# Optimization experiments

Hardware: AMD Instinct MI355X
Metric: run time of the kernel (lower is better)

Reference implementation:

```python
import jax, jax.numpy as jnp
import numpy as np

N_VARS = 50000
N_CLAUSES = 200000
E = 800000
D = 128
NFC = 3
ROUNDS = 16


def setup_inputs() -> dict:
    key = jax.random.key(0)
    ks = jax.random.split(key, 20)
    s = 0.05
    inp = {
        'L_init_w': jax.random.normal(ks[0], (D, 1)) * s,
        'L_init_b': jax.random.normal(ks[1], (D,)) * s,
        'C_init_w': jax.random.normal(ks[2], (D, 1)) * s,
        'C_init_b': jax.random.normal(ks[3], (D,)) * s,
        'Lmsg_w': jax.random.normal(ks[4], (NFC, D, D)) * s,
        'Lmsg_b': jax.random.normal(ks[5], (NFC, D)) * s,
        'Cmsg_w': jax.random.normal(ks[6], (NFC, D, D)) * s,
        'Cmsg_b': jax.random.normal(ks[7], (NFC, D)) * s,
        'Cu_wih': jax.random.normal(ks[8], (4 * D, D)) * s,
        'Cu_whh': jax.random.normal(ks[9], (4 * D, D)) * s,
        'Cu_bih': jax.random.normal(ks[10], (4 * D,)) * s,
        'Cu_bhh': jax.random.normal(ks[11], (4 * D,)) * s,
        'Lu_wih': jax.random.normal(ks[12], (4 * D, 2 * D)) * s,
        'Lu_whh': jax.random.normal(ks[13], (4 * D, D)) * s,
        'Lu_bih': jax.random.normal(ks[14], (4 * D,)) * s,
        'Lu_bhh': jax.random.normal(ks[15], (4 * D,)) * s,
        # bipartite CNF edges: src = literal index in [0, 2*n_vars), dst = local clause id in [0, n_clauses)
        'edge_src': jax.random.randint(ks[16], (E,), 0, 2 * N_VARS),
        'edge_dst': jax.random.randint(ks[17], (E,), 0, N_CLAUSES),
        'n_vars': N_VARS,
        'n_clauses': N_CLAUSES,
        'num_rounds': ROUNDS,
    }
    return inp


def _mlp(x, ws, bs):
    n = ws.shape[0]
    for i in range(n):
        x = x @ ws[i].T + bs[i]
        if i < n - 1:
            x = jax.nn.relu(x)
    return x


def _lstm(x, h, c, wih, whh, bih, bhh):
    g = x @ wih.T + h @ whh.T + bih + bhh
    i, f, gg, o = jnp.split(g, 4, axis=-1)
    c2 = jax.nn.sigmoid(f) * c + jax.nn.sigmoid(i) * jnp.tanh(gg)
    return jax.nn.sigmoid(o) * jnp.tanh(c2), c2


def reference(L_init_w, L_init_b, C_init_w, C_init_b, Lmsg_w, Lmsg_b, Cmsg_w, Cmsg_b,
              Cu_wih, Cu_whh, Cu_bih, Cu_bhh, Lu_wih, Lu_whh, Lu_bih, Lu_bhh,
              edge_src, edge_dst, n_vars, n_clauses, num_rounds):
    d = L_init_b.shape[0]
    V2 = 2 * n_vars              # literals occupy [0, V2)
    N = V2 + n_clauses           # clauses occupy [V2, N)
    l_vec = L_init_w[:, 0] + L_init_b   # L_init(ones(1))
    c_vec = C_init_w[:, 0] + C_init_b   # C_init(ones(1))
    h = jnp.concatenate([jnp.broadcast_to(l_vec, (V2, d)),
                         jnp.broadcast_to(c_vec, (n_clauses, d))], axis=0)
    c = jnp.zeros((N, d), h.dtype)

    def body(carry, _):
        h, c = carry
        # literal -> clause messages (deepset: sum of MLP(h_lit) over clause neighborhood)
        lm = _mlp(h[:V2], Lmsg_w, Lmsg_b)                          # [V2, d]
        c_msg = jax.ops.segment_sum(lm[edge_src], edge_dst, num_segments=n_clauses)
        hc, cc = _lstm(c_msg, h[V2:], c[V2:], Cu_wih, Cu_whh, Cu_bih, Cu_bhh)
        h = h.at[V2:].set(hc)
        c = c.at[V2:].set(cc)
        # clause -> literal messages (reverse direction)
        cm = _mlp(h[V2:], Cmsg_w, Cmsg_b)                          # [n_clauses, d]
        l_msg = jax.ops.segment_sum(cm[edge_dst], edge_src, num_segments=V2)
        # literal flip: state of the negated literal
        l_neg = jnp.concatenate([h[n_vars:V2], h[:n_vars]], axis=0)
        hl, cl = _lstm(jnp.concatenate([l_msg, l_neg], axis=1), h[:V2], c[:V2],
                       Lu_wih, Lu_whh, Lu_bih, Lu_bhh)
        h = h.at[:V2].set(hl)
        c = c.at[:V2].set(cl)
        return (h, c), None

    (h, c), _ = jax.lax.scan(body, (h, c), None, length=num_rounds)
    return h
```

## Files before the change

### kernel.cpp

```cpp
#include <hip/hip_runtime.h>
#include <stdint.h>

#define NVARS  50000
#define NLIT   100000
#define NCLS   200000
#define NNODE  300000
#define NEDGE  800000
#define DD     128
#define NROUNDS 16
#define NSEG   300000
#define CSRN   1600000

typedef __attribute__((ext_vector_type(8))) short   short8;
typedef __attribute__((ext_vector_type(4))) float   floatx4;

typedef __attribute__((address_space(1))) const void gvoid_t;
typedef __attribute__((address_space(3))) void       svoid_t;

static __device__ __forceinline__ float bf2f(uint16_t u){
  union { uint32_t i; float f; } v; v.i = ((uint32_t)u) << 16; return v.f;
}
static __device__ __forceinline__ uint16_t f2bf(float f){
  union { float f; uint32_t i; } v; v.f = f;
  uint32_t x = v.i;
  return (uint16_t)((x + 0x7fffu + ((x >> 16) & 1u)) >> 16);
}
static __device__ __forceinline__ float sane(float x){ return (fabsf(x) < 1e30f) ? x : 0.0f; }
static __device__ __forceinline__ float sigm(float x){ return 1.0f / (1.0f + __expf(-x)); }
static __device__ __forceinline__ float tanh_f(float x){ return 1.0f - 2.0f / (__expf(2.0f*x) + 1.0f); }

__global__ void k_init(const float* __restrict__ Lw, const float* __restrict__ Lb,
                       const float* __restrict__ Cw, const float* __restrict__ Cb,
                       uint16_t* __restrict__ hb, float* __restrict__ c32){
  long tid = (long)blockIdx.x*256 + threadIdx.x;
  if (tid >= (long)NNODE*DD) return;
  int d = (int)(tid & (DD-1));
  long i = tid >> 7;
  float v = (i < NLIT) ? (Lw[d] + Lb[d]) : (Cw[d] + Cb[d]);
  hb[tid] = f2bf(v);
  c32[tid] = 0.0f;
}

__global__ void k_setup(const float* __restrict__ Cu_wih, const float* __restrict__ Cu_whh,
                        const float* __restrict__ Cu_bih, const float* __restrict__ Cu_bhh,
                        const float* __restrict__ Lu_wih, const float* __restrict__ Lu_whh,
                        const float* __restrict__ Lu_bih, const float* __restrict__ Lu_bhh,
                        uint16_t* __restrict__ Wc, uint16_t* __restrict__ Wl,
                        float* __restrict__ bsc, float* __restrict__ bsl){
  int n = blockIdx.x;
  int t = threadIdx.x;
  Wc[n*256 + t]       = f2bf(Cu_wih[n*128 + t]);
  Wc[n*256 + 128 + t] = f2bf(Cu_whh[n*128 + t]);
  Wl[n*384 + t]       = f2bf(Lu_wih[n*256 + t]);
  Wl[n*384 + 128 + t] = f2bf(Lu_wih[n*256 + 128 + t]);
  Wl[n*384 + 256 + t] = f2bf(Lu_whh[n*128 + t]);
  if (t == 0){
    bsc[n] = Cu_bih[n] + Cu_bhh[n];
    bsl[n] = Lu_bih[n] + Lu_bhh[n];
  }
}

__global__ void k_cvtmsg(const float* __restrict__ LmW, const float* __restrict__ CmW,
                         uint16_t* __restrict__ LmWb, uint16_t* __restrict__ CmWb){
  int i = blockIdx.x*256 + threadIdx.x;
  if (i < 49152)            LmWb[i]         = f2bf(LmW[i]);
  else if (i < 2*49152)     CmWb[i - 49152] = f2bf(CmW[i - 49152]);
}

__global__ void k_hist(const int* esrc, const int* edst, int* cnt){
  int e = blockIdx.x*256 + threadIdx.x; if (e >= NEDGE) return;
  int s = esrc[e], d = edst[e];
  if ((unsigned)d < (unsigned)NCLS) atomicAdd(&cnt[d], 1);
  if ((unsigned)s < (unsigned)NLIT) atomicAdd(&cnt[NCLS + s], 1);
}

__global__ void k_reduce(const int* cnt, int* part){
  __shared__ int sm[1024];
  int i = blockIdx.x*1024 + threadIdx.x;
  sm[threadIdx.x] = (i < NSEG) ? cnt[i] : 0;
  __syncthreads();
  for (int s = 512; s > 0; s >>= 1){
    if (threadIdx.x < s) sm[threadIdx.x] += sm[threadIdx.x + s];
    __syncthreads();
  }
  if (threadIdx.x == 0) part[blockIdx.x] = sm[0];
}

__global__ void k_scanpart(int* part, int nb){
  if (blockIdx.x == 0 && threadIdx.x == 0){
    int s = 0;
    for (int b = 0; b < nb; ++b){ int v = part[b]; part[b] = s; s += v; }
  }
}

__global__ void k_scanapply(const int* cnt, const int* part, int* off, int* cur){
  __shared__ int sm[1024];
  int i = blockIdx.x*1024 + threadIdx.x;
  int v = (i < NSEG) ? cnt[i] : 0;
  sm[threadIdx.x] = v;
  __syncthreads();
  for (int s = 1; s < 1024; s <<= 1){
    int t = (threadIdx.x >= s) ? sm[threadIdx.x - s] : 0;
    __syncthreads();
    sm[threadIdx.x] += t;
    __syncthreads();
  }
  if (i < NSEG){
    int excl = part[blockIdx.x] + sm[threadIdx.x] - v;
    off[i] = excl; cur[i] = excl;
    if (i == NSEG-1) off[NSEG] = excl + v;
  }
}

__global__ void k_scatter(const int* esrc, const int* edst, int* cur, int* csr){
  int e = blockIdx.x*256 + threadIdx.x; if (e >= NEDGE) return;
  int s = esrc[e], d = edst[e];
  if ((unsigned)s < (unsigned)NLIT && (unsigned)d < (unsigned)NCLS){
    int p  = atomicAdd(&cur[d], 1);        if ((unsigned)p  < (unsigned)CSRN) csr[p]  = s;
    int p2 = atomicAdd(&cur[NCLS + s], 1); if ((unsigned)p2 < (unsigned)CSRN) csr[p2] = d;
  }
}

__global__ void k_segsum(const uint16_t* __restrict__ rows, int rowsN,
                         uint16_t* __restrict__ out,
                         const int* __restrict__ off, const int* __restrict__ csr,
                         int nseg, int segbase){
  int seg = blockIdx.x*4 + (threadIdx.x >> 6);
  if (seg >= nseg) return;
  int lane = threadIdx.x & 63;
  int s0 = off[segbase + seg], s1 = off[segbase + seg + 1];
  if (s0 < 0) s0 = 0;
  if (s1 > CSRN) s1 = CSRN;
  float ax = 0.f, ay = 0.f;
  for (int e = s0; e < s1; ++e){
    unsigned idx = (unsigned)csr[e];
    if (idx >= (unsigned)rowsN) idx = 0;
    uint32_t v = *reinterpret_cast<const uint32_t*>(rows + (size_t)idx*DD + lane*2);
    ax += bf2f((uint16_t)(v & 0xffffu));
    ay += bf2f((uint16_t)(v >> 16));
  }
  ax = sane(ax); ay = sane(ay);
  *reinterpret_cast<uint32_t*>(out + (size_t)seg*DD + lane*2) =
      (uint32_t)f2bf(ax) | ((uint32_t)f2bf(ay) << 16);
}

__global__ void __launch_bounds__(512, 4)
k_mlp3(const uint16_t* __restrict__ A, const uint16_t* __restrict__ W,
       const float* __restrict__ bias, uint16_t* __restrict__ out, int M){
  __shared__ uint16_t sX[8192];
  __shared__ uint16_t sY[8192];
  int tid  = threadIdx.x;
  int wv   = tid >> 6, lane = tid & 63;
  int mrow = lane & 15, qq = lane >> 4;
  int r0   = blockIdx.x*64;
  int slot = qq ^ ((mrow >> 1) & 3);
  int j    = wv*16 + mrow;

  short8 bfr[3][4];
#pragma unroll
  for (int l = 0; l < 3; ++l)
#pragma unroll
    for (int kt = 0; kt < 4; ++kt)
      bfr[l][kt] = *reinterpret_cast<const short8*>(
          W + (size_t)l*16384 + (size_t)j*DD + kt*32 + qq*8);

#pragma unroll
  for (int p = 0; p < 2; ++p){
    int chunk = p*512 + tid;
    int kt  = chunk >> 8;
    int row = (chunk >> 2) & 63;
    int c   = chunk & 3;
    int qc  = c ^ ((row >> 1) & 3);
    long r  = r0 + row; if (r > M-1) r = M-1;
    const uint16_t* src = A + (size_t)r*DD + kt*32 + qc*8;
    __builtin_amdgcn_global_load_lds((gvoid_t*)src,
                                     (svoid_t*)&sX[(size_t)(p*512 + wv*64)*8],
                                     16, 0, 0);
  }

  int ktj = j >> 5;
  int qcj = (j >> 3) & 3;
  __syncthreads();

  uint16_t* sIn  = sX;
  uint16_t* sOut = sY;
#pragma unroll
  for (int l = 0; l < 3; ++l){
    float bv = bias[l*128 + j];
    floatx4 acc[4];
#pragma unroll
    for (int mi = 0; mi < 4; ++mi){ floatx4 z = {0.f,0.f,0.f,0.f}; acc[mi] = z; }
#pragma unroll
    for (int kt = 0; kt < 4; ++kt)
#pragma unroll
      for (int mi = 0; mi < 4; ++mi){
        short8 af = *reinterpret_cast<const short8*>(
            &sIn[(size_t)((kt*64 + mi*16 + mrow)*4 + slot)*8]);
        acc[mi] = __builtin_amdgcn_mfma_f32_16x16x32_bf16(af, bfr[l][kt], acc[mi], 0, 0, 0);
      }
    if (l < 2){
#pragma unroll
      for (int mi = 0; mi < 4; ++mi)
#pragma unroll
        for (int r2 = 0; r2 < 4; ++r2){
          int row = mi*16 + qq*4 + r2;
          float v = sane(acc[mi][r2] + bv);
          v = v > 0.f ? v : 0.f;
          int s = qcj ^ ((row >> 1) & 3);
          sOut[(size_t)((ktj*64 + row)*4 + s)*8 + (j & 7)] = f2bf(v);
        }
      __syncthreads();
      uint16_t* t = sIn; sIn = sOut; sOut = t;
    } else {
#pragma unroll
      for (int mi = 0; mi < 4; ++mi)
#pragma unroll
        for (int r2 = 0; r2 < 4; ++r2){
          int row = r0 + mi*16 + qq*4 + r2;
          float v = sane(acc[mi][r2] + bv);
          if (row < M) out[(size_t)row*DD + j] = f2bf(v);
        }
    }
  }
}

template<int K, int NEG1>
__global__ void __launch_bounds__(512, 4)
k_lstm_fused(const uint16_t* __restrict__ A0, const uint16_t* __restrict__ A1,
             const uint16_t* __restrict__ A2,
             const uint16_t* __restrict__ W, const float* __restrict__ bias,
             float* __restrict__ c32, uint16_t* __restrict__ hout, int M){
  constexpr int NT = K/32;
  __shared__ uint16_t sW[2][16384];
  __shared__ uint16_t sA[2][2048];

  int tid  = threadIdx.x;
  int wv   = tid >> 6, lane = tid & 63;
  int mrow = lane & 15, qq = lane >> 4;
  int fb   = wv;
  int r0   = blockIdx.x*64;
  int wvu  = __builtin_amdgcn_readfirstlane(wv);

  int slot = qq ^ ((mrow >> 1) & 3);
  int sq   = (lane & 3) ^ ((lane >> 3) & 3);
  int srow = wv*16 + (lane >> 2);
  int alr  = (wv & 3)*16 + (lane >> 2);

  floatx4 acc[4][4];
#pragma unroll
  for (int i = 0; i < 4; ++i)
#pragma unroll
    for (int j = 0; j < 4; ++j){ floatx4 z = {0.f,0.f,0.f,0.f}; acc[i][j] = z; }

  auto stage = [&](int buf, int tn){
    int kt = tn*32;
#pragma unroll
    for (int c = 0; c < 4; ++c){
      const uint16_t* src = W + (size_t)(srow + c*128)*K + kt + sq*8;
      __builtin_amdgcn_global_load_lds((gvoid_t*)src,
                                       (svoid_t*)&sW[buf][wv*512 + c*4096],
                                       16, 0, 0);
    }
    if (wvu < 4){
      int rg = tn >> 2;
      const uint16_t* Ar = (rg == 0) ? A0 : ((rg == 1) ? A1 : A2);
      long gr = r0 + alr; if (gr > M-1) gr = M-1;
      if (NEG1 && rg == 1) gr = (gr < NVARS) ? gr + NVARS : gr - NVARS;
      const uint16_t* asrc = Ar + (size_t)gr*DD + (tn & 3)*32 + sq*8;
      __builtin_amdgcn_global_load_lds((gvoid_t*)asrc,
                                       (svoid_t*)&sA[buf][wv*512],
                                       16, 0, 0);
    }
  };

  stage(0, 0);
  asm volatile("s_waitcnt vmcnt(0)" ::: "memory");
  __builtin_amdgcn_sched_barrier(0);
  __builtin_amdgcn_s_barrier();
  __builtin_amdgcn_sched_barrier(0);

#pragma unroll
  for (int t = 0; t < NT; ++t){
    const int cur = t & 1;
    if (t + 1 < NT){
      stage(cur ^ 1, t + 1);
      if (wvu < 4) asm volatile("s_waitcnt vmcnt(5)" ::: "memory");
      else         asm volatile("s_waitcnt vmcnt(4)" ::: "memory");
    } else {
      asm volatile("s_waitcnt vmcnt(0)" ::: "memory");
    }
    __builtin_amdgcn_sched_barrier(0);
    __builtin_amdgcn_s_barrier();
    __builtin_amdgcn_sched_barrier(0);

    short8 af[4], bf[4];
#pragma unroll
    for (int mi = 0; mi < 4; ++mi)
      af[mi] = *reinterpret_cast<const short8*>(&sA[cur][(mi*16 + mrow)*32 + slot*8]);
#pragma unroll
    for (int gg = 0; gg < 4; ++gg)
      bf[gg] = *reinterpret_cast<const short8*>(&sW[cur][(gg*128 + fb*16 + mrow)*32 + slot*8]);
#pragma unroll
    for (int mi = 0; mi < 4; ++mi)
#pragma unroll
      for (int gg = 0; gg < 4; ++gg)
        acc[mi][gg] = __builtin_amdgcn_mfma_f32_16x16x32_bf16(af[mi], bf[gg], acc[mi][gg], 0, 0, 0);

    asm volatile("s_waitcnt lgkmcnt(0)" ::: "memory");
    __builtin_amdgcn_sched_barrier(0);
    __builtin_amdgcn_s_barrier();
    __builtin_amdgcn_sched_barrier(0);
  }

  int j = fb*16 + mrow;
  float bi = bias[j], bfv = bias[j+128], bg = bias[j+256], bo = bias[j+384];
#pragma unroll
  for (int mi = 0; mi < 4; ++mi){
    floatx4 vi = acc[mi][0], vf = acc[mi][1], vg = acc[mi][2], vo = acc[mi][3];
#pragma unroll
    for (int r2 = 0; r2 < 4; ++r2){
      int row = r0 + mi*16 + qq*4 + r2;
      if (row < M){
        size_t ix = (size_t)row*DD + j;
        float iv = sane(vi[r2] + bi);
        float fv = sane(vf[r2] + bfv);
        float gv = sane(vg[r2] + bg);
        float ov = sane(vo[r2] + bo);
        float c0 = sane(c32[ix]);
        float c2 = sigm(fv)*c0 + sigm(iv)*tanh_f(gv);
        c32[ix]  = c2;
        hout[ix] = f2bf(sigm(ov)*tanh_f(c2));
      }
    }
  }
}

__global__ void k_copy16(const uint16_t* __restrict__ src, uint16_t* __restrict__ dst, long n8){
  long i = (long)blockIdx.x*256 + threadIdx.x;
  if (i >= n8) return;
  *reinterpret_cast<ulonglong2*>(dst + i*8) =
      *reinterpret_cast<const ulonglong2*>(src + i*8);
}

__global__ void k_final(const uint16_t* __restrict__ hb, float* __restrict__ out){
  long i = (long)blockIdx.x*256 + threadIdx.x;
  if (i >= (long)NNODE*DD/4) return;
  ushort4 v = *reinterpret_cast<const ushort4*>(hb + i*4);
  float4 o;
  o.x = bf2f(v.x); o.y = bf2f(v.y); o.z = bf2f(v.z); o.w = bf2f(v.w);
  *reinterpret_cast<float4*>(out + i*4) = o;
}

extern "C" void kernel_launch(void* const* d_in, const int* in_sizes, int n_in,
                              void* d_out, int out_size, void* d_ws, size_t ws_size,
                              hipStream_t stream){
  const float* Lw     = (const float*)d_in[0];
  const float* Lb     = (const float*)d_in[1];
  const float* Cw     = (const float*)d_in[2];
  const float* Cb     = (const float*)d_in[3];
  const float* LmW    = (const float*)d_in[4];
  const float* LmB    = (const float*)d_in[5];
  const float* CmW    = (const float*)d_in[6];
  const float* CmB    = (const float*)d_in[7];
  const float* Cu_wih = (const float*)d_in[8];
  const float* Cu_whh = (const float*)d_in[9];
  const float* Cu_bih = (const float*)d_in[10];
  const float* Cu_bhh = (const float*)d_in[11];
  const float* Lu_wih = (const float*)d_in[12];
  const float* Lu_whh = (const float*)d_in[13];
  const float* Lu_bih = (const float*)d_in[14];
  const float* Lu_bhh = (const float*)d_in[15];
  const int* esrc = (const int*)d_in[16];
  const int* edst = (const int*)d_in[17];

  char* p = (char*)d_ws;
  auto alloc = [&](size_t bytes)->char* {
    char* r = p; p += (bytes + 255) & ~(size_t)255; return r;
  };
  int* cnt  = (int*)alloc((size_t)NSEG*4);
  int* off  = (int*)alloc((size_t)(NSEG+1)*4);
  int* cur  = (int*)alloc((size_t)NSEG*4);
  int nb = (NSEG + 1023) / 1024;
  int* part = (int*)alloc((size_t)nb*4);
  int* csr  = (int*)alloc((size_t)CSRN*4);
  uint16_t* Wc   = (uint16_t*)alloc((size_t)512*256*2);
  uint16_t* Wl   = (uint16_t*)alloc((size_t)512*384*2);
  uint16_t* LmWb = (uint16_t*)alloc((size_t)3*128*128*2);
  uint16_t* CmWb = (uint16_t*)alloc((size_t)3*128*128*2);
  float* bsc = (float*)alloc(512*4);
  float* bsl = (float*)alloc(512*4);
  uint16_t* t0 = (uint16_t*)alloc((size_t)NCLS*DD*2);
  uint16_t* t1 = (uint16_t*)alloc((size_t)NCLS*DD*2);
  uint16_t* hb = (uint16_t*)alloc((size_t)NNODE*DD*2);

  float* c32 = (float*)d_out;
  uint16_t* hbC = hb  + (size_t)NLIT*DD;
  float*    cL  = c32;
  float*    cC  = c32 + (size_t)NLIT*DD;

  hipMemsetAsync(cnt, 0, (size_t)NSEG*4, stream);
  k_init<<<(NNODE*DD + 255)/256, 256, 0, stream>>>(Lw, Lb, Cw, Cb, hb, c32);
  k_setup<<<512, 128, 0, stream>>>(Cu_wih, Cu_whh, Cu_bih, Cu_bhh,
                                   Lu_wih, Lu_whh, Lu_bih, Lu_bhh,
                                   Wc, Wl, bsc, bsl);
  k_cvtmsg<<<(2*49152 + 255)/256, 256, 0, stream>>>(LmW, CmW, LmWb, CmWb);
  k_hist<<<(NEDGE + 255)/256, 256, 0, stream>>>(esrc, edst, cnt);
  k_reduce<<<nb, 1024, 0, stream>>>(cnt, part);
  k_scanpart<<<1, 64, 0, stream>>>(part, nb);
  k_scanapply<<<nb, 1024, 0, stream>>>(cnt, part, off, cur);
  k_scatter<<<(NEDGE + 255)/256, 256, 0, stream>>>(esrc, edst, cur, csr);

  for (int rd = 0; rd < NROUNDS; ++rd){
    k_mlp3<<<1563, 512, 0, stream>>>(hb, LmWb, LmB, t0, NLIT);
    k_segsum<<<50000, 256, 0, stream>>>(t0, NLIT, t1, off, csr, NCLS, 0);
    k_lstm_fused<256,0><<<3125, 512, 0, stream>>>(t1, hbC, nullptr, Wc, bsc, cC, hbC, NCLS);
    k_mlp3<<<3125, 512, 0, stream>>>(hbC, CmWb, CmB, t0, NCLS);
    k_segsum<<<25000, 256, 0, stream>>>(t0, NCLS, t1, off, csr, NLIT, NCLS);
    k_copy16<<<6250, 256, 0, stream>>>(hb, t0, (long)NLIT*DD/8);
    k_lstm_fused<384,1><<<1563, 512, 0, stream>>>(t1, t0, t0, Wl, bsl, cL, hb, NLIT);
  }

  k_final<<<(NNODE*DD/4 + 255)/256, 256, 0, stream>>>(hb, (float*)d_out);
}
```

Before: 9.488 ms.

## Pair literal and negation rows in LSTM tile; keep clause LSTM weights in registers

The literal LSTM kernel now gives each block 32 variables plus their 32 negated literals. The negation input is then always a row inside the same block's update set, so the per-round copy of literal h into a scratch buffer is dropped and the kernel reads and writes hb in place. The clause LSTM kernel drops its LDS double-buffered pipeline and keeps its full weight slice in registers, loading activations straight from global memory. The in-place update assumes no block reads rows another block writes, which this pairing ensures. The register-resident weights raise register pressure, and the launch-bounds occupancy hint drops from 4 to 2.

```diff
diff --git a/kernel.cpp b/kernel.cpp
--- a/kernel.cpp
+++ b/kernel.cpp
@@ -224,93 +224,53 @@
   }
 }
 
-template<int K, int NEG1>
-__global__ void __launch_bounds__(512, 4)
-k_lstm_fused(const uint16_t* __restrict__ A0, const uint16_t* __restrict__ A1,
-             const uint16_t* __restrict__ A2,
-             const uint16_t* __restrict__ W, const float* __restrict__ bias,
-             float* __restrict__ c32, uint16_t* __restrict__ hout, int M){
-  constexpr int NT = K/32;
-  __shared__ uint16_t sW[2][16384];
-  __shared__ uint16_t sA[2][2048];
-
+__global__ void __launch_bounds__(512, 2)
+k_lstm_cls(const uint16_t* __restrict__ A0, const uint16_t* __restrict__ A1,
+           const uint16_t* __restrict__ W, const float* __restrict__ bias,
+           float* __restrict__ c32, uint16_t* __restrict__ hout, int M){
   int tid  = threadIdx.x;
   int wv   = tid >> 6, lane = tid & 63;
   int mrow = lane & 15, qq = lane >> 4;
   int fb   = wv;
   int r0   = blockIdx.x*64;
-  int wvu  = __builtin_amdgcn_readfirstlane(wv);
-
-  int slot = qq ^ ((mrow >> 1) & 3);
-  int sq   = (lane & 3) ^ ((lane >> 3) & 3);
-  int srow = wv*16 + (lane >> 2);
-  int alr  = (wv & 3)*16 + (lane >> 2);
+
+  short8 breg[4][8];
+#pragma unroll
+  for (int gg = 0; gg < 4; ++gg)
+#pragma unroll
+    for (int t = 0; t < 8; ++t)
+      breg[gg][t] = *reinterpret_cast<const short8*>(
+          W + (size_t)(gg*128 + fb*16 + mrow)*256 + t*32 + qq*8);
+
+  const uint16_t* ap[2][4];
+#pragma unroll
+  for (int mi = 0; mi < 4; ++mi){
+    int r = r0 + mi*16 + mrow; if (r > M-1) r = M-1;
+    ap[0][mi] = A0 + (size_t)r*DD + qq*8;
+    ap[1][mi] = A1 + (size_t)r*DD + qq*8;
+  }
 
   floatx4 acc[4][4];
 #pragma unroll
   for (int i = 0; i < 4; ++i)
 #pragma unroll
-    for (int j = 0; j < 4; ++j){ floatx4 z = {0.f,0.f,0.f,0.f}; acc[i][j] = z; }
-
-  auto stage = [&](int buf, int tn){
-    int kt = tn*32;
-#pragma unroll
-    for (int c = 0; c < 4; ++c){
-      const uint16_t* src = W + (size_t)(srow + c*128)*K + kt + sq*8;
-      __builtin_amdgcn_global_load_lds((gvoid_t*)src,
-                                       (svoid_t*)&sW[buf][wv*512 + c*4096],
-                                       16, 0, 0);
-    }
-    if (wvu < 4){
-      int rg = tn >> 2;
-      const uint16_t* Ar = (rg == 0) ? A0 : ((rg == 1) ? A1 : A2);
-      long gr = r0 + alr; if (gr > M-1) gr = M-1;
-      if (NEG1 && rg == 1) gr = (gr < NVARS) ? gr + NVARS : gr - NVARS;
-      const uint16_t* asrc = Ar + (size_t)gr*DD + (tn & 3)*32 + sq*8;
-      __builtin_amdgcn_global_load_lds((gvoid_t*)asrc,
-                                       (svoid_t*)&sA[buf][wv*512],
-                                       16, 0, 0);
-    }
-  };
-
-  stage(0, 0);
-  asm volatile("s_waitcnt vmcnt(0)" ::: "memory");
-  __builtin_amdgcn_sched_barrier(0);
-  __builtin_amdgcn_s_barrier();
-  __builtin_amdgcn_sched_barrier(0);
-
-#pragma unroll
-  for (int t = 0; t < NT; ++t){
-    const int cur = t & 1;
-    if (t + 1 < NT){
-      stage(cur ^ 1, t + 1);
-      if (wvu < 4) asm volatile("s_waitcnt vmcnt(5)" ::: "memory");
-      else         asm volatile("s_waitcnt vmcnt(4)" ::: "memory");
-    } else {
-      asm volatile("s_waitcnt vmcnt(0)" ::: "memory");
-    }
-    __builtin_amdgcn_sched_barrier(0);
-    __builtin_amdgcn_s_barrier();
-    __builtin_amdgcn_sched_barrier(0);
-
-    short8 af[4], bf[4];
+    for (int j2 = 0; j2 < 4; ++j2){ floatx4 z = {0.f,0.f,0.f,0.f}; acc[i][j2] = z; }
+
+#pragma unroll
+  for (int t = 0; t < 8; ++t){
+    const int rg = t >> 2, ko = (t & 3)*32;
+    short8 af[4];
 #pragma unroll
     for (int mi = 0; mi < 4; ++mi)
-      af[mi] = *reinterpret_cast<const short8*>(&sA[cur][(mi*16 + mrow)*32 + slot*8]);
-#pragma unroll
-    for (int gg = 0; gg < 4; ++gg)
-      bf[gg] = *reinterpret_cast<const short8*>(&sW[cur][(gg*128 + fb*16 + mrow)*32 + slot*8]);
+      af[mi] = *reinterpret_cast<const short8*>(ap[rg][mi] + ko);
 #pragma unroll
     for (int mi = 0; mi < 4; ++mi)
 #pragma unroll
       for (int gg = 0; gg < 4; ++gg)
-        acc[mi][gg] = __builtin_amdgcn_mfma_f32_16x16x32_bf16(af[mi], bf[gg], acc[mi][gg], 0, 0, 0);
-
-    asm volatile("s_waitcnt lgkmcnt(0)" ::: "memory");
-    __builtin_amdgcn_sched_barrier(0);
-    __builtin_amdgcn_s_barrier();
-    __builtin_amdgcn_sched_barrier(0);
-  }
+        acc[mi][gg] = __builtin_amdgcn_mfma_f32_16x16x32_bf16(af[mi], breg[gg][t], acc[mi][gg], 0, 0, 0);
+  }
+
+  __syncthreads();
 
   int j = fb*16 + mrow;
   float bi = bias[j], bfv = bias[j+128], bg = bias[j+256], bo = bias[j+384];
@@ -335,11 +295,122 @@
   }
 }
 
-__global__ void k_copy16(const uint16_t* __restrict__ src, uint16_t* __restrict__ dst, long n8){
-  long i = (long)blockIdx.x*256 + threadIdx.x;
-  if (i >= n8) return;
-  *reinterpret_cast<ulonglong2*>(dst + i*8) =
-      *reinterpret_cast<const ulonglong2*>(src + i*8);
+__global__ void __launch_bounds__(512, 4)
+k_lstm_lit(const uint16_t* __restrict__ A0, const uint16_t* __restrict__ hbl,
+           const uint16_t* __restrict__ W, const float* __restrict__ bias,
+           float* __restrict__ c32, uint16_t* __restrict__ hout){
+  constexpr int NT = 12;
+  __shared__ uint16_t sW[2][16384];
+  __shared__ uint16_t sA[2][2048];
+
+  int tid  = threadIdx.x;
+  int wv   = tid >> 6, lane = tid & 63;
+  int mrow = lane & 15, qq = lane >> 4;
+  int fb   = wv;
+  long base = (long)blockIdx.x*32;
+  int wvu  = __builtin_amdgcn_readfirstlane(wv);
+
+  int slot = qq ^ ((mrow >> 1) & 3);
+  int sq   = (lane & 3) ^ ((lane >> 3) & 3);
+  int srow = wv*16 + (lane >> 2);
+  int alr  = (wv & 3)*16 + (lane >> 2);
+
+  auto pmap = [&](int lr)->long {
+    long g = (lr < 32) ? base + lr : (long)NVARS + base + (lr - 32);
+    long cap = (lr < 32) ? (long)NVARS - 1 : (long)NLIT - 1;
+    return g > cap ? cap : g;
+  };
+
+  floatx4 acc[4][4];
+#pragma unroll
+  for (int i = 0; i < 4; ++i)
+#pragma unroll
+    for (int j2 = 0; j2 < 4; ++j2){ floatx4 z = {0.f,0.f,0.f,0.f}; acc[i][j2] = z; }
+
+  auto stage = [&](int buf, int tn){
+    int kt = tn*32;
+#pragma unroll
+    for (int c = 0; c < 4; ++c){
+      const uint16_t* src = W + (size_t)(srow + c*128)*384 + kt + sq*8;
+      __builtin_amdgcn_global_load_lds((gvoid_t*)src,
+                                       (svoid_t*)&sW[buf][wv*512 + c*4096],
+                                       16, 0, 0);
+    }
+    if (wvu < 4){
+      int rg = tn >> 2;
+      int lr = (rg == 1) ? ((alr + 32) & 63) : alr;
+      long gr = pmap(lr);
+      const uint16_t* Ar = (rg == 0) ? A0 : hbl;
+      const uint16_t* asrc = Ar + (size_t)gr*DD + (tn & 3)*32 + sq*8;
+      __builtin_amdgcn_global_load_lds((gvoid_t*)asrc,
+                                       (svoid_t*)&sA[buf][wv*512],
+                                       16, 0, 0);
+    }
+  };
+
+  stage(0, 0);
+  asm volatile("s_waitcnt vmcnt(0)" ::: "memory");
+  __builtin_amdgcn_sched_barrier(0);
+  __builtin_amdgcn_s_barrier();
+  __builtin_amdgcn_sched_barrier(0);
+
+#pragma unroll
+  for (int t = 0; t < NT; ++t){
+    const int cur = t & 1;
+    if (t + 1 < NT){
+      stage(cur ^ 1, t + 1);
+      if (wvu < 4) asm volatile("s_waitcnt vmcnt(5)" ::: "memory");
+      else         asm volatile("s_waitcnt vmcnt(4)" ::: "memory");
+    } else {
+      asm volatile("s_waitcnt vmcnt(0)" ::: "memory");
+    }
+    __builtin_amdgcn_sched_barrier(0);
+    __builtin_amdgcn_s_barrier();
+    __builtin_amdgcn_sched_barrier(0);
+
+    short8 af[4], bf[4];
+#pragma unroll
+    for (int mi = 0; mi < 4; ++mi)
+      af[mi] = *reinterpret_cast<const short8*>(&sA[cur][(mi*16 + mrow)*32 + slot*8]);
+#pragma unroll
+    for (int gg = 0; gg < 4; ++gg)
+      bf[gg] = *reinterpret_cast<const short8*>(&sW[cur][(gg*128 + fb*16 + mrow)*32 + slot*8]);
+#pragma unroll
+    for (int mi = 0; mi < 4; ++mi)
+#pragma unroll
+      for (int gg = 0; gg < 4; ++gg)
+        acc[mi][gg] = __builtin_amdgcn_mfma_f32_16x16x32_bf16(af[mi], bf[gg], acc[mi][gg], 0, 0, 0);
+
+    asm volatile("s_waitcnt lgkmcnt(0)" ::: "memory");
+    __builtin_amdgcn_sched_barrier(0);
+    __builtin_amdgcn_s_barrier();
+    __builtin_amdgcn_sched_barrier(0);
+  }
+
+  int j = fb*16 + mrow;
+  float bi = bias[j], bfv = bias[j+128], bg = bias[j+256], bo = bias[j+384];
+#pragma unroll
+  for (int mi = 0; mi < 4; ++mi){
+    floatx4 vi = acc[mi][0], vf = acc[mi][1], vg = acc[mi][2], vo = acc[mi][3];
+#pragma unroll
+    for (int r2 = 0; r2 < 4; ++r2){
+      int lrow = mi*16 + qq*4 + r2;
+      bool valid = (lrow < 32) ? (base + lrow < NVARS)
+                               : (base + (lrow - 32) < NVARS);
+      if (valid){
+        long grow = (lrow < 32) ? base + lrow : (long)NVARS + base + (lrow - 32);
+        size_t ix = (size_t)grow*DD + j;
+        float iv = sane(vi[r2] + bi);
+        float fv = sane(vf[r2] + bfv);
+        float gv = sane(vg[r2] + bg);
+        float ov = sane(vo[r2] + bo);
+        float c0 = sane(c32[ix]);
+        float c2 = sigm(fv)*c0 + sigm(iv)*tanh_f(gv);
+        c32[ix]  = c2;
+        hout[ix] = f2bf(sigm(ov)*tanh_f(c2));
+      }
+    }
+  }
 }
 
 __global__ void k_final(const uint16_t* __restrict__ hb, float* __restrict__ out){
@@ -413,11 +484,10 @@
   for (int rd = 0; rd < NROUNDS; ++rd){
     k_mlp3<<<1563, 512, 0, stream>>>(hb, LmWb, LmB, t0, NLIT);
     k_segsum<<<50000, 256, 0, stream>>>(t0, NLIT, t1, off, csr, NCLS, 0);
-    k_lstm_fused<256,0><<<3125, 512, 0, stream>>>(t1, hbC, nullptr, Wc, bsc, cC, hbC, NCLS);
+    k_lstm_cls<<<3125, 512, 0, stream>>>(t1, hbC, Wc, bsc, cC, hbC, NCLS);
     k_mlp3<<<3125, 512, 0, stream>>>(hbC, CmWb, CmB, t0, NCLS);
     k_segsum<<<25000, 256, 0, stream>>>(t0, NCLS, t1, off, csr, NLIT, NCLS);
-    k_copy16<<<6250, 256, 0, stream>>>(hb, t0, (long)NLIT*DD/8);
-    k_lstm_fused<384,1><<<1563, 512, 0, stream>>>(t1, t0, t0, Wl, bsl, cL, hb, NLIT);
+    k_lstm_lit<<<1563, 512, 0, stream>>>(t1, hb, Wl, bsl, cL, hb);
   }
 
   k_final<<<(NNODE*DD/4 + 255)/256, 256, 0, stream>>>(hb, (float*)d_out);
```

New measurement: 11.83 ms. 1.25x slower.

## Double LSTM row tile and pair literals with negations to drop the h copy

Applied to the files above, without the earlier changes.

The fused LSTM kernel now computes 128 rows per block instead of 64. This halves how often the gate weight tiles are reloaded per row, and all eight waves now load activations. For the literal update, each block handles variable rows base..base+63 together with their negated counterparts at NVARS+base. Every block therefore reads only the h rows it writes, so h can be updated in place and the per-round copy kernel is removed. The cost is roughly double the accumulator registers and lower occupancy (launch bound 2), plus fewer blocks in the grid.

```diff
diff --git a/kernel.cpp b/kernel.cpp
--- a/kernel.cpp
+++ b/kernel.cpp
@@ -224,33 +224,54 @@
   }
 }
 
-template<int K, int NEG1>
-__global__ void __launch_bounds__(512, 4)
-k_lstm_fused(const uint16_t* __restrict__ A0, const uint16_t* __restrict__ A1,
-             const uint16_t* __restrict__ A2,
-             const uint16_t* __restrict__ W, const float* __restrict__ bias,
-             float* __restrict__ c32, uint16_t* __restrict__ hout, int M){
+template<int K, int LIT>
+__global__ void __launch_bounds__(512, 2)
+k_lstm2(const uint16_t* __restrict__ A0, const uint16_t* __restrict__ H,
+        const uint16_t* __restrict__ W, const float* __restrict__ bias,
+        float* __restrict__ c32, uint16_t* __restrict__ hout, int M){
   constexpr int NT = K/32;
+  constexpr int NR = K/128;
   __shared__ uint16_t sW[2][16384];
-  __shared__ uint16_t sA[2][2048];
+  __shared__ uint16_t sA[2][4096];
 
   int tid  = threadIdx.x;
   int wv   = tid >> 6, lane = tid & 63;
   int mrow = lane & 15, qq = lane >> 4;
   int fb   = wv;
-  int r0   = blockIdx.x*64;
-  int wvu  = __builtin_amdgcn_readfirstlane(wv);
-
   int slot = qq ^ ((mrow >> 1) & 3);
   int sq   = (lane & 3) ^ ((lane >> 3) & 3);
   int srow = wv*16 + (lane >> 2);
-  int alr  = (wv & 3)*16 + (lane >> 2);
-
-  floatx4 acc[4][4];
-#pragma unroll
-  for (int i = 0; i < 4; ++i)
-#pragma unroll
-    for (int j = 0; j < 4; ++j){ floatx4 z = {0.f,0.f,0.f,0.f}; acc[i][j] = z; }
+  int alr  = wv*16 + (lane >> 2);
+
+  long r0   = LIT ? 0 : (long)blockIdx.x*128;
+  long base = LIT ? (long)blockIdx.x*64 : 0;
+
+  const uint16_t* pA[NR];
+  {
+    if constexpr (!LIT){
+      long gr = r0 + alr; if (gr > M-1) gr = M-1;
+      pA[0] = A0 + (size_t)gr*DD + sq*8;
+      pA[1] = H  + (size_t)gr*DD + sq*8;
+    } else {
+      int lr = alr;
+      long g  = (lr < 64) ? base + lr : (long)NVARS + base + (lr - 64);
+      long gc = (lr < 64) ? (long)NVARS - 1 : (long)NLIT - 1;
+      if (g > gc) g = gc;
+      int ln  = (lr + 64) & 127;
+      long gn  = (ln < 64) ? base + ln : (long)NVARS + base + (ln - 64);
+      long gnc = (ln < 64) ? (long)NVARS - 1 : (long)NLIT - 1;
+      if (gn > gnc) gn = gnc;
+      pA[0] = A0 + (size_t)g*DD  + sq*8;
+      pA[1] = H  + (size_t)gn*DD + sq*8;
+      pA[2] = H  + (size_t)g*DD  + sq*8;
+    }
+  }
+
+  floatx4 acc[8][4];
+#pragma unroll
+  for (int i = 0; i < 8; ++i)
+#pragma unroll
+    for (int j2 = 0; j2 < 4; ++j2){ floatx4 z = {0.f,0.f,0.f,0.f}; acc[i][j2] = z; }
 
   auto stage = [&](int buf, int tn){
     int kt = tn*32;
@@ -261,16 +282,11 @@
                                        (svoid_t*)&sW[buf][wv*512 + c*4096],
                                        16, 0, 0);
     }
-    if (wvu < 4){
-      int rg = tn >> 2;
-      const uint16_t* Ar = (rg == 0) ? A0 : ((rg == 1) ? A1 : A2);
-      long gr = r0 + alr; if (gr > M-1) gr = M-1;
-      if (NEG1 && rg == 1) gr = (gr < NVARS) ? gr + NVARS : gr - NVARS;
-      const uint16_t* asrc = Ar + (size_t)gr*DD + (tn & 3)*32 + sq*8;
-      __builtin_amdgcn_global_load_lds((gvoid_t*)asrc,
-                                       (svoid_t*)&sA[buf][wv*512],
-                                       16, 0, 0);
-    }
+    const int rg = tn >> 2;
+    const uint16_t* asrc = pA[rg] + (tn & 3)*32;
+    __builtin_amdgcn_global_load_lds((gvoid_t*)asrc,
+                                     (svoid_t*)&sA[buf][wv*512],
+                                     16, 0, 0);
   };
 
   stage(0, 0);
@@ -284,8 +300,7 @@
     const int cur = t & 1;
     if (t + 1 < NT){
       stage(cur ^ 1, t + 1);
-      if (wvu < 4) asm volatile("s_waitcnt vmcnt(5)" ::: "memory");
-      else         asm volatile("s_waitcnt vmcnt(4)" ::: "memory");
+      asm volatile("s_waitcnt vmcnt(5)" ::: "memory");
     } else {
       asm volatile("s_waitcnt vmcnt(0)" ::: "memory");
     }
@@ -293,15 +308,15 @@
     __builtin_amdgcn_s_barrier();
     __builtin_amdgcn_sched_barrier(0);
 
-    short8 af[4], bf[4];
-#pragma unroll
-    for (int mi = 0; mi < 4; ++mi)
+    short8 af[8], bf[4];
+#pragma unroll
+    for (int mi = 0; mi < 8; ++mi)
       af[mi] = *reinterpret_cast<const short8*>(&sA[cur][(mi*16 + mrow)*32 + slot*8]);
 #pragma unroll
     for (int gg = 0; gg < 4; ++gg)
       bf[gg] = *reinterpret_cast<const short8*>(&sW[cur][(gg*128 + fb*16 + mrow)*32 + slot*8]);
 #pragma unroll
-    for (int mi = 0; mi < 4; ++mi)
+    for (int mi = 0; mi < 8; ++mi)
 #pragma unroll
       for (int gg = 0; gg < 4; ++gg)
         acc[mi][gg] = __builtin_amdgcn_mfma_f32_16x16x32_bf16(af[mi], bf[gg], acc[mi][gg], 0, 0, 0);
@@ -315,13 +330,21 @@
   int j = fb*16 + mrow;
   float bi = bias[j], bfv = bias[j+128], bg = bias[j+256], bo = bias[j+384];
 #pragma unroll
-  for (int mi = 0; mi < 4; ++mi){
+  for (int mi = 0; mi < 8; ++mi){
     floatx4 vi = acc[mi][0], vf = acc[mi][1], vg = acc[mi][2], vo = acc[mi][3];
 #pragma unroll
     for (int r2 = 0; r2 < 4; ++r2){
-      int row = r0 + mi*16 + qq*4 + r2;
-      if (row < M){
-        size_t ix = (size_t)row*DD + j;
+      int lrow = mi*16 + qq*4 + r2;
+      long grow; bool valid;
+      if constexpr (!LIT){
+        grow = r0 + lrow; valid = grow < M;
+      } else {
+        valid = (lrow < 64) ? (base + lrow < NVARS)
+                            : (base + (lrow - 64) < NVARS);
+        grow  = (lrow < 64) ? base + lrow : (long)NVARS + base + (lrow - 64);
+      }
+      if (valid){
+        size_t ix = (size_t)grow*DD + j;
         float iv = sane(vi[r2] + bi);
         float fv = sane(vf[r2] + bfv);
         float gv = sane(vg[r2] + bg);
@@ -333,13 +356,6 @@
       }
     }
   }
-}
-
-__global__ void k_copy16(const uint16_t* __restrict__ src, uint16_t* __restrict__ dst, long n8){
-  long i = (long)blockIdx.x*256 + threadIdx.x;
-  if (i >= n8) return;
-  *reinterpret_cast<ulonglong2*>(dst + i*8) =
-      *reinterpret_cast<const ulonglong2*>(src + i*8);
 }
 
 __global__ void k_final(const uint16_t* __restrict__ hb, float* __restrict__ out){
@@ -413,11 +429,10 @@
   for (int rd = 0; rd < NROUNDS; ++rd){
     k_mlp3<<<1563, 512, 0, stream>>>(hb, LmWb, LmB, t0, NLIT);
     k_segsum<<<50000, 256, 0, stream>>>(t0, NLIT, t1, off, csr, NCLS, 0);
-    k_lstm_fused<256,0><<<3125, 512, 0, stream>>>(t1, hbC, nullptr, Wc, bsc, cC, hbC, NCLS);
+    k_lstm2<256,0><<<1563, 512, 0, stream>>>(t1, hbC, Wc, bsc, cC, hbC, NCLS);
     k_mlp3<<<3125, 512, 0, stream>>>(hbC, CmWb, CmB, t0, NCLS);
     k_segsum<<<25000, 256, 0, stream>>>(t0, NCLS, t1, off, csr, NLIT, NCLS);
-    k_copy16<<<6250, 256, 0, stream>>>(hb, t0, (long)NLIT*DD/8);
-    k_lstm_fused<384,1><<<1563, 512, 0, stream>>>(t1, t0, t0, Wl, bsl, cL, hb, NLIT);
+    k_lstm2<384,1><<<782, 512, 0, stream>>>(t1, hb, Wl, bsl, cL, hb, NLIT);
   }
 
   k_final<<<(NNODE*DD/4 + 255)/256, 256, 0, stream>>>(hb, (float*)d_out);
```

After: 10.76 ms. 1.13x slower.
